# Optimization experiments

Hardware: AMD Instinct MI355X
Metric: run time of the kernel (lower is better)

Reference implementation:

```python
import jax, jax.numpy as jnp
import numpy as np

H = 50  # hidden_size

def setup_inputs() -> dict:
    key = jax.random.key(0)
    ks = jax.random.split(key, 7)
    B, T = 2048, 1024
    s = 1.0 / np.sqrt(H)  # PyTorch default init scale
    return {
        "x": jax.random.normal(ks[0], (B, T, 1), dtype=jnp.float32),
        "W_ih": jax.random.uniform(ks[1], (4 * H, 1), jnp.float32, -s, s),
        "W_hh": jax.random.uniform(ks[2], (4 * H, H), jnp.float32, -s, s),
        "b_ih": jax.random.uniform(ks[3], (4 * H,), jnp.float32, -s, s),
        "b_hh": jax.random.uniform(ks[4], (4 * H,), jnp.float32, -s, s),
        "W_lin": jax.random.uniform(ks[5], (1, H), jnp.float32, -s, s),
        "b_lin": jax.random.uniform(ks[6], (1,), jnp.float32, -s, s),
    }

def reference(x, W_ih, W_hh, b_ih, b_hh, W_lin, b_lin):
    B, T, _ = x.shape
    # Precompute input contribution to gates for all timesteps: [T, B, 4H]
    gx = jnp.einsum('bti,gi->tbg', x, W_ih) + (b_ih + b_hh)

    def step(carry, gx_t):
        h, c = carry
        gates = gx_t + h @ W_hh.T               # [B, 4H]
        i, f, g, o = jnp.split(gates, 4, axis=-1)  # PyTorch gate order i,f,g,o
        i = jax.nn.sigmoid(i)
        f = jax.nn.sigmoid(f)
        g = jnp.tanh(g)
        o = jax.nn.sigmoid(o)
        c = f * c + i * g
        h = o * jnp.tanh(c)
        return (h, c), None

    h0 = jnp.zeros((B, H), x.dtype)
    c0 = jnp.zeros((B, H), x.dtype)
    (h_last, _), _ = jax.lax.scan(step, (h0, c0), gx)
    # Linear head on last timestep's hidden state -> [B, 1]
    return h_last @ W_lin.T + b_lin
```

## Files before the change

### kernel.cpp

```cpp
#include <hip/hip_runtime.h>


#define H     50
#define TT    1024
#define BATCH 2048
#define BW    8
#define NTHR  448
#define KP    80
#define KX_HI 56
#define KX_LO 57
#define KX_H2 58
#define KB_HI 59
#define KB_LO 60

typedef float    f32x4 __attribute__((ext_vector_type(4)));
typedef _Float16 f16x8 __attribute__((ext_vector_type(8)));

__global__ __launch_bounds__(NTHR, 1) void lstm_kernel(
    const float* __restrict__ x,
    const float* __restrict__ W_ih,
    const float* __restrict__ W_hh,
    const float* __restrict__ b_ih,
    const float* __restrict__ b_hh,
    const float* __restrict__ W_lin,
    const float* __restrict__ b_lin,
    float* __restrict__ out)
{
    __shared__ _Float16 hb[2][BW][KP];
    __shared__ float    redH[H][BW];

    const int tid  = threadIdx.x;
    const int wave = tid >> 6;
    const int lane = tid & 63;
    const int L15  = lane & 15;
    const int kq   = lane >> 4;
    const int bl   = L15 & 7;
    const int b0   = blockIdx.x * BW;

    const int t0 = 2 * wave;

    const float LOG2E  = 1.4426950408889634f;
    const float LOG2E2 = 2.8853900817779268f;

    f16x8 A[2][2];
    #pragma unroll
    for (int tt = 0; tt < 2; ++tt) {
        const int m  = (t0 + tt) * 16 + L15;
        const int jm = m >> 2, gm = m & 3;
        const bool v = (jm < H);
        const float s = (gm == 2) ? LOG2E2 : -LOG2E;
        float swih = 0.f, sbias = 0.f;
        if (v) {
            swih  = s * W_ih[gm * H + jm];
            sbias = s * (b_ih[gm * H + jm] + b_hh[gm * H + jm]);
        }
        const _Float16 whi = (_Float16)swih;
        const _Float16 wlo = (_Float16)(swih - (float)whi);
        const _Float16 bhi = (_Float16)sbias;
        const _Float16 blo = (_Float16)(sbias - (float)bhi);
        #pragma unroll
        for (int kf = 0; kf < 2; ++kf) {
            f16x8 vv;
            #pragma unroll
            for (int e = 0; e < 8; ++e) {
                const int k = kf * 32 + kq * 8 + e;
                _Float16 val = (_Float16)0.f;
                if (v) {
                    if (k < H)            val = (_Float16)(s * W_hh[(gm * H + jm) * H + k]);
                    else if (k == KX_HI)  val = whi;
                    else if (k == KX_LO)  val = whi;
                    else if (k == KX_H2)  val = wlo;
                    else if (k == KB_HI)  val = bhi;
                    else if (k == KB_LO)  val = blo;
                }
                vv[e] = val;
            }
            A[tt][kf] = vv;
        }
    }

    const int  j  = 8 * wave + ((L15 >> 3) << 2) + kq;
    const bool jv = (j < H);
    const float wlin = jv ? W_lin[j] : 0.f;

    for (int i = tid; i < 2 * BW * KP; i += NTHR)
        ((_Float16*)hb)[i] = (_Float16)0.f;
    __syncthreads();
    if (tid < 16) {
        hb[tid >> 3][tid & 7][KB_HI] = (_Float16)1.0f;
        hb[tid >> 3][tid & 7][KB_LO] = (_Float16)1.0f;
    } else if (tid < 24) {
        const int bb = tid - 16;
        const float xv = x[(size_t)(b0 + bb) * TT];
        const _Float16 xh = (_Float16)xv;
        hb[0][bb][KX_HI] = xh;
        hb[0][bb][KX_LO] = (_Float16)(xv - (float)xh);
        hb[0][bb][KX_H2] = xh;
    }

    const float* xrow = x + (size_t)(b0 + bl) * TT;
    float4 xq = {0,0,0,0}, xq2 = {0,0,0,0};
    const bool xw = (wave >= 1 && wave <= 3);
    if (xw) {
        xq  = *(const float4*)(xrow);
        xq2 = *(const float4*)(xrow + 4);
    }
    const int xslot = (wave == 1) ? KX_HI : (wave == 2) ? KX_LO : KX_H2;

    float c = 0.f, hlast = 0.f;
    __syncthreads();

    for (int t = 0; t < TT; ++t) {
        const _Float16* hp = &hb[t & 1][bl][0];
        f16x8 B0 = *(const f16x8*)(hp + kq * 8);
        f16x8 B1 = *(const f16x8*)(hp + 32 + kq * 8);

        const f32x4 z = {0.f, 0.f, 0.f, 0.f};
        f32x4 a0 = __builtin_amdgcn_mfma_f32_16x16x32_f16(A[0][0], B0, z, 0, 0, 0);
        f32x4 a1 = __builtin_amdgcn_mfma_f32_16x16x32_f16(A[1][0], B0, z, 0, 0, 0);
        a0 = __builtin_amdgcn_mfma_f32_16x16x32_f16(A[0][1], B1, a0, 0, 0, 0);
        a1 = __builtin_amdgcn_mfma_f32_16x16x32_f16(A[1][1], B1, a1, 0, 0, 0);

        const int idx = t + 1;
        const int nb  = idx & 1;

        if (xw) {
            if ((idx & 3) == 0) {
                xq = xq2;
                int o = idx + 4; if (o > TT - 4) o = TT - 4;
                xq2 = *(const float4*)(xrow + o);
            }
            if (L15 < 8 && kq == 0) {
                const float xv = ((const float*)&xq)[idx & 3];
                const _Float16 xh = (_Float16)xv;
                const _Float16 wv = (wave == 2) ? (_Float16)(xv - (float)xh) : xh;
                hb[nb][L15][xslot] = wv;
            }
        }

        const bool lo = (L15 < 8);
        const float gi = lo ? a0[0] : a1[0];
        const float gf = lo ? a0[1] : a1[1];
        const float gg = lo ? a0[2] : a1[2];
        const float go = lo ? a0[3] : a1[3];

        const float Ei = __builtin_amdgcn_exp2f(gi);
        const float Ef = __builtin_amdgcn_exp2f(gf);
        const float Eg = __builtin_amdgcn_exp2f(gg);
        const float Eo = __builtin_amdgcn_exp2f(go);
        const float P  = (1.0f + Ei) * (1.0f + Eg);
        const float Q  = 1.0f + Ef;
        const float num = __builtin_fmaf(c, P, (Eg - 1.0f) * Q);
        c = num * __builtin_amdgcn_rcpf(P * Q);
        const float ca = fminf(LOG2E2 * c, 80.0f);
        const float Ec = __builtin_amdgcn_exp2f(ca);
        const float h  = (Ec - 1.0f) *
            __builtin_amdgcn_rcpf((1.0f + Eo) * (1.0f + Ec));
        hlast = h;

        hb[nb][bl][j] = (_Float16)h;
        __syncthreads();
    }

    if (jv && L15 < 8) redH[j][bl] = wlin * hlast;
    else if (jv)       redH[j][bl] = wlin * hlast;
    __syncthreads();
    if (tid < BW) {
        float s = b_lin[0];
        #pragma unroll 10
        for (int jj = 0; jj < H; ++jj) s += redH[jj][tid];
        out[b0 + tid] = s;
    }
}

extern "C" void kernel_launch(void* const* d_in, const int* in_sizes, int n_in,
                              void* d_out, int out_size, void* d_ws, size_t ws_size,
                              hipStream_t stream) {
    const float* x     = (const float*)d_in[0];
    const float* W_ih  = (const float*)d_in[1];
    const float* W_hh  = (const float*)d_in[2];
    const float* b_ih  = (const float*)d_in[3];
    const float* b_hh  = (const float*)d_in[4];
    const float* W_lin = (const float*)d_in[5];
    const float* b_lin = (const float*)d_in[6];
    float* out = (float*)d_out;

    dim3 grid(BATCH / BW);
    dim3 block(NTHR);
    lstm_kernel<<<grid, block, 0, stream>>>(x, W_ih, W_hh, b_ih, b_hh,
                                            W_lin, b_lin, out);
}
```

Measured before the change: 364.1 us.

## Preload x into LDS as packed fp16 hi/lo and splice into MFMA operand

All x values for the block's 8 sequences are read up front and stored in shared memory as packed fp16 hi/lo pairs. Each step then builds the second B operand in registers, inserting the x and bias-one entries directly for the kq==3 lanes, instead of having dedicated waves write x into the h buffer every step. The time loop is also unrolled by two so the buffer parity is fixed at compile time. This removes per-step global loads and the conditional x-write path from the critical recurrence, at the cost of 32KB of extra LDS and a longer prologue.

```diff
diff --git a/kernel.cpp b/kernel.cpp
--- a/kernel.cpp
+++ b/kernel.cpp
@@ -7,14 +7,10 @@
 #define BW    8
 #define NTHR  448
 #define KP    80
-#define KX_HI 56
-#define KX_LO 57
-#define KX_H2 58
-#define KB_HI 59
-#define KB_LO 60
 
-typedef float    f32x4 __attribute__((ext_vector_type(4)));
-typedef _Float16 f16x8 __attribute__((ext_vector_type(8)));
+typedef float        f32x4 __attribute__((ext_vector_type(4)));
+typedef _Float16     f16x8 __attribute__((ext_vector_type(8)));
+typedef unsigned int u32x4 __attribute__((ext_vector_type(4)));
 
 __global__ __launch_bounds__(NTHR, 1) void lstm_kernel(
     const float* __restrict__ x,
@@ -26,8 +22,9 @@
     const float* __restrict__ b_lin,
     float* __restrict__ out)
 {
-    __shared__ _Float16 hb[2][BW][KP];
-    __shared__ float    redH[H][BW];
+    __shared__ _Float16     hb[2][BW][KP];
+    __shared__ unsigned int XT[TT][BW];
+    __shared__ float        redH[H][BW];
 
     const int tid  = threadIdx.x;
     const int wave = tid >> 6;
@@ -66,12 +63,12 @@
                 const int k = kf * 32 + kq * 8 + e;
                 _Float16 val = (_Float16)0.f;
                 if (v) {
-                    if (k < H)            val = (_Float16)(s * W_hh[(gm * H + jm) * H + k]);
-                    else if (k == KX_HI)  val = whi;
-                    else if (k == KX_LO)  val = whi;
-                    else if (k == KX_H2)  val = wlo;
-                    else if (k == KB_HI)  val = bhi;
-                    else if (k == KB_LO)  val = blo;
+                    if (k < H)        val = (_Float16)(s * W_hh[(gm * H + jm) * H + k]);
+                    else if (k == 56) val = whi;
+                    else if (k == 57) val = whi;
+                    else if (k == 58) val = wlo;
+                    else if (k == 59) val = bhi;
+                    else if (k == 60) val = blo;
                 }
                 vv[e] = val;
             }
@@ -82,88 +79,72 @@
     const int  j  = 8 * wave + ((L15 >> 3) << 2) + kq;
     const bool jv = (j < H);
     const float wlin = jv ? W_lin[j] : 0.f;
+    const bool k3 = (kq == 3);
 
     for (int i = tid; i < 2 * BW * KP; i += NTHR)
         ((_Float16*)hb)[i] = (_Float16)0.f;
-    __syncthreads();
-    if (tid < 16) {
-        hb[tid >> 3][tid & 7][KB_HI] = (_Float16)1.0f;
-        hb[tid >> 3][tid & 7][KB_LO] = (_Float16)1.0f;
-    } else if (tid < 24) {
-        const int bb = tid - 16;
-        const float xv = x[(size_t)(b0 + bb) * TT];
+    for (int i = tid; i < TT * BW; i += NTHR) {
+        const int bb = i >> 10, t = i & 1023;
+        const float xv = x[(size_t)(b0 + bb) * TT + t];
         const _Float16 xh = (_Float16)xv;
-        hb[0][bb][KX_HI] = xh;
-        hb[0][bb][KX_LO] = (_Float16)(xv - (float)xh);
-        hb[0][bb][KX_H2] = xh;
+        const _Float16 xl = (_Float16)(xv - (float)xh);
+        XT[t][bb] = (unsigned int)*(const unsigned short*)&xh |
+                    ((unsigned int)*(const unsigned short*)&xl << 16);
     }
-
-    const float* xrow = x + (size_t)(b0 + bl) * TT;
-    float4 xq = {0,0,0,0}, xq2 = {0,0,0,0};
-    const bool xw = (wave >= 1 && wave <= 3);
-    if (xw) {
-        xq  = *(const float4*)(xrow);
-        xq2 = *(const float4*)(xrow + 4);
-    }
-    const int xslot = (wave == 1) ? KX_HI : (wave == 2) ? KX_LO : KX_H2;
 
     float c = 0.f, hlast = 0.f;
     __syncthreads();
 
-    for (int t = 0; t < TT; ++t) {
-        const _Float16* hp = &hb[t & 1][bl][0];
-        f16x8 B0 = *(const f16x8*)(hp + kq * 8);
-        f16x8 B1 = *(const f16x8*)(hp + 32 + kq * 8);
+    #pragma unroll 1
+    for (int tbase = 0; tbase < TT; tbase += 2) {
+        #pragma unroll
+        for (int half = 0; half < 2; ++half) {
+            const int t = tbase + half;
+            const _Float16* hp = &hb[half][bl][0];
+            _Float16*       np = &hb[half ^ 1][bl][0];
 
-        const f32x4 z = {0.f, 0.f, 0.f, 0.f};
-        f32x4 a0 = __builtin_amdgcn_mfma_f32_16x16x32_f16(A[0][0], B0, z, 0, 0, 0);
-        f32x4 a1 = __builtin_amdgcn_mfma_f32_16x16x32_f16(A[1][0], B0, z, 0, 0, 0);
-        a0 = __builtin_amdgcn_mfma_f32_16x16x32_f16(A[0][1], B1, a0, 0, 0, 0);
-        a1 = __builtin_amdgcn_mfma_f32_16x16x32_f16(A[1][1], B1, a1, 0, 0, 0);
+            f16x8 B0 = *(const f16x8*)(hp + kq * 8);
+            u32x4 Bh = *(const u32x4*)(hp + 32 + kq * 8);
+            const unsigned int xt = XT[t][bl];
+            u32x4 Bm;
+            Bm[0] = k3 ? xt : Bh[0];
+            Bm[1] = k3 ? ((xt & 0xFFFFu) | 0x3C000000u) : Bh[1];
+            Bm[2] = k3 ? 0x00003C00u : Bh[2];
+            Bm[3] = k3 ? 0u : Bh[3];
+            const f16x8 B1 = __builtin_bit_cast(f16x8, Bm);
 
-        const int idx = t + 1;
-        const int nb  = idx & 1;
+            const f32x4 z = {0.f, 0.f, 0.f, 0.f};
+            f32x4 a0 = __builtin_amdgcn_mfma_f32_16x16x32_f16(A[0][0], B0, z, 0, 0, 0);
+            f32x4 a1 = __builtin_amdgcn_mfma_f32_16x16x32_f16(A[1][0], B0, z, 0, 0, 0);
+            a0 = __builtin_amdgcn_mfma_f32_16x16x32_f16(A[0][1], B1, a0, 0, 0, 0);
+            a1 = __builtin_amdgcn_mfma_f32_16x16x32_f16(A[1][1], B1, a1, 0, 0, 0);
 
-        if (xw) {
-            if ((idx & 3) == 0) {
-                xq = xq2;
-                int o = idx + 4; if (o > TT - 4) o = TT - 4;
-                xq2 = *(const float4*)(xrow + o);
-            }
-            if (L15 < 8 && kq == 0) {
-                const float xv = ((const float*)&xq)[idx & 3];
-                const _Float16 xh = (_Float16)xv;
-                const _Float16 wv = (wave == 2) ? (_Float16)(xv - (float)xh) : xh;
-                hb[nb][L15][xslot] = wv;
-            }
+            const bool lo = (L15 < 8);
+            const float gi = lo ? a0[0] : a1[0];
+            const float gf = lo ? a0[1] : a1[1];
+            const float gg = lo ? a0[2] : a1[2];
+            const float go = lo ? a0[3] : a1[3];
+
+            const float Ei = __builtin_amdgcn_exp2f(gi);
+            const float Ef = __builtin_amdgcn_exp2f(gf);
+            const float Eg = __builtin_amdgcn_exp2f(gg);
+            const float Eo = __builtin_amdgcn_exp2f(go);
+            const float P  = (1.0f + Ei) * (1.0f + Eg);
+            const float Q  = 1.0f + Ef;
+            const float num = __builtin_fmaf(c, P, (Eg - 1.0f) * Q);
+            c = num * __builtin_amdgcn_rcpf(P * Q);
+            const float ca = fminf(LOG2E2 * c, 80.0f);
+            const float Ec = __builtin_amdgcn_exp2f(ca);
+            const float h  = (Ec - 1.0f) *
+                __builtin_amdgcn_rcpf((1.0f + Eo) * (1.0f + Ec));
+            hlast = h;
+
+            np[j] = (_Float16)h;
+            __syncthreads();
         }
-
-        const bool lo = (L15 < 8);
-        const float gi = lo ? a0[0] : a1[0];
-        const float gf = lo ? a0[1] : a1[1];
-        const float gg = lo ? a0[2] : a1[2];
-        const float go = lo ? a0[3] : a1[3];
-
-        const float Ei = __builtin_amdgcn_exp2f(gi);
-        const float Ef = __builtin_amdgcn_exp2f(gf);
-        const float Eg = __builtin_amdgcn_exp2f(gg);
-        const float Eo = __builtin_amdgcn_exp2f(go);
-        const float P  = (1.0f + Ei) * (1.0f + Eg);
-        const float Q  = 1.0f + Ef;
-        const float num = __builtin_fmaf(c, P, (Eg - 1.0f) * Q);
-        c = num * __builtin_amdgcn_rcpf(P * Q);
-        const float ca = fminf(LOG2E2 * c, 80.0f);
-        const float Ec = __builtin_amdgcn_exp2f(ca);
-        const float h  = (Ec - 1.0f) *
-            __builtin_amdgcn_rcpf((1.0f + Eo) * (1.0f + Ec));
-        hlast = h;
-
-        hb[nb][bl][j] = (_Float16)h;
-        __syncthreads();
     }
 
-    if (jv && L15 < 8) redH[j][bl] = wlin * hlast;
-    else if (jv)       redH[j][bl] = wlin * hlast;
+    if (jv) redH[j][bl] = wlin * hlast;
     __syncthreads();
     if (tid < BW) {
         float s = b_lin[0];
```

New measurement: 344.9 us. -5.3%, faster.
